# Optimization experiments

Measured on AMD Instinct MI355X. Metric: run time of the kernel, lower is better.

## Reference

```python
import jax, jax.numpy as jnp
import numpy as np

B, OP, MA, F_IN, F_OUT = 8, 400, 200, 64, 64


def setup_inputs() -> dict:
    key = jax.random.key(0)
    ks = jax.random.split(key, 8)
    x = jax.random.normal(ks[0], (B, OP, F_IN), dtype=jnp.float32)
    y = jax.random.normal(ks[1], (B, MA, F_IN), dtype=jnp.float32)
    z = jax.random.normal(ks[2], (B, OP, MA, F_IN), dtype=jnp.float32)
    op_ma_adj = jax.random.randint(ks[3], (B, OP, MA), 0, 2, dtype=jnp.int32)
    # xavier-uniform-ish params
    lim = float(np.sqrt(6.0 / (F_IN + F_OUT)))
    W_op = jax.random.uniform(ks[4], (F_IN, F_OUT), minval=-lim, maxval=lim, dtype=jnp.float32)
    W_ma = jax.random.uniform(ks[5], (F_IN, F_OUT), minval=-lim, maxval=lim, dtype=jnp.float32)
    W_edge = jax.random.uniform(ks[6], (F_IN, F_OUT), minval=-lim, maxval=lim, dtype=jnp.float32)
    lim_a = float(np.sqrt(6.0 / (1 + 3 * F_OUT)))
    att_vec = jax.random.uniform(ks[7], (3 * F_OUT,), minval=-lim_a, maxval=lim_a, dtype=jnp.float32)
    return {"x": x, "y": y, "z": z, "op_ma_adj": op_ma_adj,
            "W_op": W_op, "W_ma": W_ma, "W_edge": W_edge, "att_vec": att_vec}


def reference(x, y, z, op_ma_adj, W_op, W_ma, W_edge, att_vec):
    F = W_op.shape[1]
    h_op = jnp.einsum('bni,io->bno', x, W_op)                      # [B, op, F]
    h = jnp.einsum('bmi,io->bmo', y, W_ma)                         # [B, ma, F]
    h_edge = jnp.einsum('bnmi,io->bnmo', z, W_edge).transpose(0, 2, 1, 3)  # [B, ma, op, F]
    # attention score: concat([h_op, h_ma, h_edge]) @ a  ==  per-part dot products (no BxMAxOPx3F materialization)
    a_op, a_ma, a_edge = att_vec[:F], att_vec[F:2 * F], att_vec[2 * F:]
    e = (jnp.einsum('bnf,f->bn', h_op, a_op)[:, None, :]
         + jnp.einsum('bmf,f->bm', h, a_ma)[:, :, None]
         + jnp.einsum('bmnf,f->bmn', h_edge, a_edge))              # [B, ma, op]
    e = jax.nn.leaky_relu(e, negative_slope=0.01)
    adjT = op_ma_adj.transpose(0, 2, 1)                            # [B, ma, op]
    row_empty = jnp.all(adjT == 0, axis=-1, keepdims=True)         # [B, ma, 1]
    att = jnp.where(adjT > 0, e, -jnp.inf)
    att = jnp.where(row_empty, 0.0, att)                           # empty rows -> uniform softmax (matches torch)
    att = jax.nn.softmax(att, axis=-1)                             # [B, ma, op]
    h_op_edge = h_op[:, None, :, :] + h_edge                       # [B, ma, op, F]
    h_prime = jnp.einsum('bmn,bmnf->bmf', att, h_op_edge)          # [B, ma, F]
    h_prime = jnp.where(row_empty, 0.0, h_prime) + h
    return jax.nn.elu(h_prime)
```

## Files before the change

kernel.cpp:

```cpp
#include <hip/hip_runtime.h>
#include <math.h>

#define B_   8
#define OP_  400
#define MA_  200
#define NCH  4
#define CH   100
#define RPW  25
#define PSTR 132
#define NEGM -1.0e30f

__global__ __launch_bounds__(256) void precompute_k(
    const float* __restrict__ x, const float* __restrict__ y,
    const float* __restrict__ Wop, const float* __restrict__ Wma,
    const float* __restrict__ Wedge, const float* __restrict__ att,
    float* __restrict__ ws_we, float* __restrict__ ws_eop, float* __restrict__ ws_ema)
{
    __shared__ float w_s[192];
    const int tid = threadIdx.x, wv = tid >> 6, ln = tid & 63;
    if (tid < 192) {
        const int which = tid >> 6, i = tid & 63;
        const float* W = (which == 0) ? Wop : ((which == 1) ? Wma : Wedge);
        const float* a = att + which * 64;
        float acc = 0.f;
        #pragma unroll 8
        for (int f = 0; f < 64; ++f) acc = fmaf(W[i * 64 + f], a[f], acc);
        w_s[tid] = acc;
    }
    __syncthreads();
    if (blockIdx.x == 0 && tid < 64) ws_we[tid] = w_s[128 + tid];

    const int row = blockIdx.x * 4 + wv;
    if (row < B_ * OP_) {
        float s = x[(size_t)row * 64 + ln] * w_s[ln];
        #pragma unroll
        for (int o = 32; o > 0; o >>= 1) s += __shfl_xor(s, o, 64);
        if (ln == 0) ws_eop[row] = s;
    } else if (row < B_ * OP_ + B_ * MA_) {
        const int r2 = row - B_ * OP_;
        float s = y[(size_t)r2 * 64 + ln] * w_s[64 + ln];
        #pragma unroll
        for (int o = 32; o > 0; o >>= 1) s += __shfl_xor(s, o, 64);
        if (ln == 0) ws_ema[r2] = s;
    }
}

__global__ __launch_bounds__(256) void gat_chunk(
    const float* __restrict__ x, const float* __restrict__ z,
    const int* __restrict__ adj,
    const float* __restrict__ ws_we, const float* __restrict__ ws_eop,
    const float* __restrict__ ws_ema, float* __restrict__ part)
{
    __shared__ int   act[CH];
    __shared__ float s_arr[CH];
    __shared__ float red[8];
    __shared__ float vred[4][64];
    __shared__ float ured[4][64];

    const int tid = threadIdx.x, wv = tid >> 6, ln = tid & 63;
    const int blk = blockIdx.x;
    const int bm = blk / NCH, c = blk % NCH;
    const int b = bm / MA_, m = bm % MA_;
    const int n0 = c * CH;
    const int nbase = wv * RPW;

    if (tid < CH) {
        const int n = n0 + tid;
        act[tid]   = adj[((size_t)(b * OP_ + n)) * MA_ + m];
        s_arr[tid] = NEGM;
    }
    const float wel = ws_we[ln];
    const float ema = ws_ema[bm];
    __syncthreads();

    const float* zb = z + ((size_t)(b * OP_ + n0) * MA_ + m) * 64;
    const float* xb = x + (size_t)(b * OP_ + n0) * 64;
    float zreg[RPW], xreg[RPW];
    #pragma unroll
    for (int i = 0; i < RPW; ++i) {
        const int n = nbase + i;
        const bool a = (act[n] != 0);
        zreg[i] = a ? zb[(size_t)n * (MA_ * 64) + ln] : 0.f;
        xreg[i] = a ? xb[(size_t)n * 64 + ln]         : 0.f;
    }

    #pragma unroll
    for (int i = 0; i < RPW; ++i) {
        const int n = nbase + i;
        if (act[n] != 0) {
            float s = zreg[i] * wel;
            #pragma unroll
            for (int o = 32; o > 0; o >>= 1) s += __shfl_xor(s, o, 64);
            if (ln == 0) {
                float e = s + ws_eop[b * OP_ + n0 + n] + ema;
                s_arr[n] = (e >= 0.f) ? e : 0.01f * e;
            }
        }
    }
    __syncthreads();

    float lm = NEGM;
    for (int n = tid; n < CH; n += 256) lm = fmaxf(lm, s_arr[n]);
    #pragma unroll
    for (int o = 32; o > 0; o >>= 1) lm = fmaxf(lm, __shfl_xor(lm, o, 64));
    if (ln == 0) red[wv] = lm;
    __syncthreads();
    const float M = fmaxf(fmaxf(red[0], red[1]), fmaxf(red[2], red[3]));

    float ls = 0.f;
    for (int n = tid; n < CH; n += 256) {
        const float p = (act[n] != 0) ? __expf(s_arr[n] - M) : 0.f;
        s_arr[n] = p;
        ls += p;
    }
    #pragma unroll
    for (int o = 32; o > 0; o >>= 1) ls += __shfl_xor(ls, o, 64);
    if (ln == 0) red[4 + wv] = ls;
    __syncthreads();
    const float L = red[4] + red[5] + red[6] + red[7];

    float v = 0.f, u = 0.f;
    #pragma unroll
    for (int i = 0; i < RPW; ++i) {
        const int n = nbase + i;
        if (act[n] != 0) {
            const float p = s_arr[n];
            v = fmaf(p, zreg[i], v);
            u = fmaf(p, xreg[i], u);
        }
    }
    vred[wv][ln] = v; ured[wv][ln] = u;
    __syncthreads();

    float* pp = part + (size_t)blk * PSTR;
    if (tid < 64)        pp[tid] = vred[0][tid] + vred[1][tid] + vred[2][tid] + vred[3][tid];
    else if (tid < 128)  pp[tid] = ured[0][tid-64] + ured[1][tid-64] + ured[2][tid-64] + ured[3][tid-64];
    else if (tid == 128) { pp[128] = M; pp[129] = L; }
}

__global__ __launch_bounds__(256) void gat_combine(
    const float* __restrict__ y,
    const float* __restrict__ Wop, const float* __restrict__ Wma,
    const float* __restrict__ Wedge,
    const float* __restrict__ part, float* __restrict__ out)
{
    __shared__ float vs[4][64], us[4][64], ys[4][64];
    const int tid = threadIdx.x, wv = tid >> 6, ln = tid & 63;
    const int row = blockIdx.x * 4 + wv;

    const float* pp = part + (size_t)row * NCH * PSTR;
    float M = NEGM;
    #pragma unroll
    for (int c = 0; c < NCH; ++c) M = fmaxf(M, pp[c * PSTR + 128]);
    float L = 0.f, v = 0.f, u = 0.f;
    #pragma unroll
    for (int c = 0; c < NCH; ++c) {
        const float Mc = pp[c * PSTR + 128];
        const float w  = (Mc > -1.0e29f) ? __expf(Mc - M) : 0.f;
        L += w * pp[c * PSTR + 129];
        v += w * pp[c * PSTR + ln];
        u += w * pp[c * PSTR + 64 + ln];
    }
    const float inv = (L > 0.f) ? (1.f / L) : 0.f;
    vs[wv][ln] = v * inv;
    us[wv][ln] = u * inv;
    ys[wv][ln] = y[(size_t)row * 64 + ln];
    __syncthreads();

    float hv = 0.f;
    #pragma unroll 8
    for (int i = 0; i < 64; ++i) {
        hv += vs[wv][i] * Wedge[i * 64 + ln]
            + us[wv][i] * Wop[i * 64 + ln]
            + ys[wv][i] * Wma[i * 64 + ln];
    }
    out[(size_t)row * 64 + ln] = (hv > 0.f) ? hv : (__expf(hv) - 1.f);
}

extern "C" void kernel_launch(void* const* d_in, const int* in_sizes, int n_in,
                              void* d_out, int out_size, void* d_ws, size_t ws_size,
                              hipStream_t stream) {
    const float* x     = (const float*)d_in[0];
    const float* y     = (const float*)d_in[1];
    const float* z     = (const float*)d_in[2];
    const int*   adj   = (const int*)d_in[3];
    const float* Wop   = (const float*)d_in[4];
    const float* Wma   = (const float*)d_in[5];
    const float* Wedge = (const float*)d_in[6];
    const float* att   = (const float*)d_in[7];

    float* ws     = (float*)d_ws;
    float* ws_we  = ws;
    float* ws_eop = ws + 64;
    float* ws_ema = ws + 64 + B_ * OP_;
    float* part   = ws + 64 + B_ * OP_ + B_ * MA_;

    precompute_k<<<1200, 256, 0, stream>>>(
        x, y, Wop, Wma, Wedge, att, ws_we, ws_eop, ws_ema);
    gat_chunk<<<B_ * MA_ * NCH, 256, 0, stream>>>(
        x, z, adj, ws_we, ws_eop, ws_ema, part);
    gat_combine<<<(B_ * MA_) / 4, 256, 0, stream>>>(
        y, Wop, Wma, Wedge, part, (float*)d_out);
}
```

Before: 276.0 us.

## Compute edge scores with float4 row loads and drop register caching of z/x

Computes the per-edge score with four lanes per row, each loading 16 floats as float4. Rows are processed 16 per wave pass in two passes, and only a 2-step shuffle reduction is needed instead of a 6-step one per row. The z and x rows are no longer held in registers across the softmax; they are re-read from global memory in the weighted-sum phase. This lowers register pressure and shuffle count but reads z twice, relying on cache hits for the second read.

```diff
diff --git a/kernel.cpp b/kernel.cpp
--- a/kernel.cpp
+++ b/kernel.cpp
@@ -51,11 +51,12 @@
     const float* __restrict__ ws_we, const float* __restrict__ ws_eop,
     const float* __restrict__ ws_ema, float* __restrict__ part)
 {
-    __shared__ int   act[CH];
-    __shared__ float s_arr[CH];
-    __shared__ float red[8];
-    __shared__ float vred[4][64];
-    __shared__ float ured[4][64];
+    __shared__ int    act[CH];
+    __shared__ float  s_arr[CH];
+    __shared__ float  red[8];
+    __shared__ float4 we4[16];
+    __shared__ float  vred[4][64];
+    __shared__ float  ured[4][64];
 
     const int tid = threadIdx.x, wv = tid >> 6, ln = tid & 63;
     const int blk = blockIdx.x;
@@ -69,32 +70,36 @@
         act[tid]   = adj[((size_t)(b * OP_ + n)) * MA_ + m];
         s_arr[tid] = NEGM;
     }
-    const float wel = ws_we[ln];
+    if (tid < 64) ((float*)we4)[tid] = ws_we[tid];
     const float ema = ws_ema[bm];
     __syncthreads();
 
     const float* zb = z + ((size_t)(b * OP_ + n0) * MA_ + m) * 64;
     const float* xb = x + (size_t)(b * OP_ + n0) * 64;
-    float zreg[RPW], xreg[RPW];
-    #pragma unroll
-    for (int i = 0; i < RPW; ++i) {
-        const int n = nbase + i;
-        const bool a = (act[n] != 0);
-        zreg[i] = a ? zb[(size_t)n * (MA_ * 64) + ln] : 0.f;
-        xreg[i] = a ? xb[(size_t)n * 64 + ln]         : 0.f;
-    }
-
-    #pragma unroll
-    for (int i = 0; i < RPW; ++i) {
-        const int n = nbase + i;
-        if (act[n] != 0) {
-            float s = zreg[i] * wel;
-            #pragma unroll
-            for (int o = 32; o > 0; o >>= 1) s += __shfl_xor(s, o, 64);
-            if (ln == 0) {
-                float e = s + ws_eop[b * OP_ + n0 + n] + ema;
-                s_arr[n] = (e >= 0.f) ? e : 0.01f * e;
-            }
+
+    const int r = ln >> 2, g = ln & 3;
+    const float4 w0 = we4[g * 4 + 0], w1 = we4[g * 4 + 1];
+    const float4 w2 = we4[g * 4 + 2], w3 = we4[g * 4 + 3];
+    #pragma unroll
+    for (int batch = 0; batch < 2; ++batch) {
+        const int lrow = batch * 16 + r;
+        const bool valid = (lrow < RPW);
+        const int n = nbase + (valid ? lrow : 0);
+        const bool a = valid && (act[n] != 0);
+        float s = 0.f;
+        if (a) {
+            const float4* zr = (const float4*)(zb + (size_t)n * (MA_ * 64) + g * 16);
+            float4 q0 = zr[0], q1 = zr[1], q2 = zr[2], q3 = zr[3];
+            s = fmaf(q0.x, w0.x, fmaf(q0.y, w0.y, fmaf(q0.z, w0.z, q0.w * w0.w)));
+            s = fmaf(q1.x, w1.x, fmaf(q1.y, w1.y, fmaf(q1.z, w1.z, fmaf(q1.w, w1.w, s))));
+            s = fmaf(q2.x, w2.x, fmaf(q2.y, w2.y, fmaf(q2.z, w2.z, fmaf(q2.w, w2.w, s))));
+            s = fmaf(q3.x, w3.x, fmaf(q3.y, w3.y, fmaf(q3.z, w3.z, fmaf(q3.w, w3.w, s))));
+        }
+        s += __shfl_xor(s, 1, 64);
+        s += __shfl_xor(s, 2, 64);
+        if (a && g == 0) {
+            float e = s + ws_eop[b * OP_ + n0 + n] + ema;
+            s_arr[n] = (e >= 0.f) ? e : 0.01f * e;
         }
     }
     __syncthreads();
@@ -125,8 +130,8 @@
         const int n = nbase + i;
         if (act[n] != 0) {
             const float p = s_arr[n];
-            v = fmaf(p, zreg[i], v);
-            u = fmaf(p, xreg[i], u);
+            v = fmaf(p, zb[(size_t)n * (MA_ * 64) + ln], v);
+            u = fmaf(p, xb[(size_t)n * 64 + ln], u);
         }
     }
     vred[wv][ln] = v; ured[wv][ln] = u;
```

New measurement: 261.9 us. 5.1% less time.
